# Performance work log

Hardware: AMD Instinct MI355X
Metric: run time of the kernel (lower is better)

Reference implementation:

```python
import jax, jax.numpy as jnp
import numpy as np

N_NODES = 100000
N_EDGES = 1000000
D_FEAT = 64          # per-node embedding dim
IN_FEATS = 2 * D_FEAT  # concat(src, dst)
HID = 128


def setup_inputs() -> dict:
    key = jax.random.key(0)
    ks = jax.random.split(key, 12)
    zi = jax.random.normal(ks[0], (N_NODES, D_FEAT), dtype=jnp.float32)
    zj = jax.random.normal(ks[1], (N_NODES, D_FEAT), dtype=jnp.float32)
    zn = jax.random.normal(ks[2], (N_NODES, D_FEAT), dtype=jnp.float32)
    pos_src = jax.random.randint(ks[3], (N_EDGES,), 0, N_NODES)
    pos_dst = jax.random.randint(ks[4], (N_EDGES,), 0, N_NODES)
    neg_src = jax.random.randint(ks[5], (N_EDGES,), 0, N_NODES)
    neg_dst = jax.random.randint(ks[6], (N_EDGES,), 0, N_NODES)
    # MLP params (nn.Linear style: y = x @ W.T + b)
    s1 = 1.0 / np.sqrt(IN_FEATS)
    s3 = 1.0 / np.sqrt(HID)
    W1 = jax.random.uniform(ks[7], (HID, IN_FEATS), jnp.float32, -s1, s1)
    b1 = jax.random.uniform(ks[8], (HID,), jnp.float32, -s1, s1)
    W3 = jax.random.uniform(ks[9], (1, HID), jnp.float32, -s3, s3)
    b3 = jax.random.uniform(ks[10], (1,), jnp.float32, -s3, s3)
    return {"zi": zi, "zj": zj, "zn": zn, "W1": W1, "b1": b1, "W3": W3,
            "b3": b3, "pos_src": pos_src, "pos_dst": pos_dst,
            "neg_src": neg_src, "neg_dst": neg_dst}


def _lp(raw, W1, b1, W3, b3):
    # Link_Prediction with n_layers=2, dropout=0: linear-relu-linear-sigmoid
    hid = jax.nn.relu(raw @ W1.T + b1)      # [E, HID]
    return jax.nn.sigmoid(hid @ W3.T + b3)  # [E, 1]


def reference(zi, zj, zn, W1, b1, W3, b3, pos_src, pos_dst, neg_src, neg_dst):
    # pos graph: gather src/dst node embeddings per edge, concat -> MLP
    raw_pos = jnp.concatenate([zi[pos_src], zj[pos_dst]], axis=1)  # [E, 2*D]
    pos_score = _lp(raw_pos, W1, b1, W3, b3)
    # NOTE: source bug — neg score is computed from the POS raw features
    # (pos_graph.edata['raw']); the neg gather/concat is dead code, so we
    # faithfully score raw_pos again.
    neg_score = _lp(raw_pos, W1, b1, W3, b3)
    return pos_score, neg_score
```

## Files before the change

### kernel.cpp

```cpp
#include <hip/hip_runtime.h>

typedef float    f32x16 __attribute__((ext_vector_type(16)));
typedef _Float16 f16x8  __attribute__((ext_vector_type(8)));

#define NWAVES 4
#define TPW 4
#define TILES_PER_BLOCK (NWAVES * TPW)

__global__ __launch_bounds__(256) void prep_f16(
    const float* __restrict__ zi, const float* __restrict__ zj,
    _Float16* __restrict__ zif, _Float16* __restrict__ zjf, const int nChunkPer)
{
    const int stride = gridDim.x * blockDim.x;
    for (int c = blockIdx.x * blockDim.x + threadIdx.x; c < 2 * nChunkPer; c += stride) {
        const float* s;
        _Float16* d;
        if (c < nChunkPer) { s = zi + (size_t)c * 8; d = zif + (size_t)c * 8; }
        else { s = zj + (size_t)(c - nChunkPer) * 8; d = zjf + (size_t)(c - nChunkPer) * 8; }
        const float4 a0 = *reinterpret_cast<const float4*>(s);
        const float4 a1 = *reinterpret_cast<const float4*>(s + 4);
        f16x8 v;
        v[0]=(_Float16)a0.x; v[1]=(_Float16)a0.y; v[2]=(_Float16)a0.z; v[3]=(_Float16)a0.w;
        v[4]=(_Float16)a1.x; v[5]=(_Float16)a1.y; v[6]=(_Float16)a1.z; v[7]=(_Float16)a1.w;
        *reinterpret_cast<f16x8*>(d) = v;
    }
}

template<bool F16TAB>
__global__ __launch_bounds__(256) void graphlp_mfma(
    const float* __restrict__ zi, const float* __restrict__ zj,
    const _Float16* __restrict__ zif, const _Float16* __restrict__ zjf,
    const float* __restrict__ W1, const float* __restrict__ b1p,
    const float* __restrict__ W3, const float* __restrict__ b3p,
    const int* __restrict__ psrc, const int* __restrict__ pdst,
    float* __restrict__ out, const int nEdges, const int nTiles)
{
    __shared__ uint4 w1s[2048];
    char* lds = reinterpret_cast<char*>(w1s);
    const int tid = threadIdx.x;

    #pragma unroll
    for (int i = 0; i < 8; ++i) {
        const int ch  = tid + i * 256;
        const int row = ch >> 4;
        const int kg  = ch & 15;
        const float* s = W1 + row * 128 + kg * 8;
        const float4 a0 = *reinterpret_cast<const float4*>(s);
        const float4 a1 = *reinterpret_cast<const float4*>(s + 4);
        f16x8 v;
        v[0]=(_Float16)a0.x; v[1]=(_Float16)a0.y; v[2]=(_Float16)a0.z; v[3]=(_Float16)a0.w;
        v[4]=(_Float16)a1.x; v[5]=(_Float16)a1.y; v[6]=(_Float16)a1.z; v[7]=(_Float16)a1.w;
        const int off = row * 256 + ((kg * 16) ^ ((row & 7) << 4));
        *reinterpret_cast<f16x8*>(lds + off) = v;
    }
    __syncthreads();

    const int lane = tid & 63;
    const int wav  = tid >> 6;
    const int lr   = lane & 31;
    const int lq   = lane >> 5;

    float b1v[4], w3v[4];
    #pragma unroll
    for (int nb = 0; nb < 4; ++nb) {
        b1v[nb] = b1p[nb * 32 + lr];
        w3v[nb] = W3[nb * 32 + lr];
    }
    const float b3 = b3p[0];

    int si = 0, di = 0;
    {
        const int g0 = blockIdx.x * TILES_PER_BLOCK + wav;
        if (g0 < nTiles) {
            const int e = min(g0 * 32 + lr, nEdges - 1);
            si = psrc[e]; di = pdst[e];
        }
    }

    for (int t = 0; t < TPW; ++t) {
        const int g = blockIdx.x * TILES_PER_BLOCK + t * NWAVES + wav;
        if (g >= nTiles) break;

        int si_n = 0, di_n = 0;
        if (t + 1 < TPW) {
            const int gn = g + NWAVES;
            if (gn < nTiles) {
                const int en = min(gn * 32 + lr, nEdges - 1);
                si_n = psrc[en]; di_n = pdst[en];
            }
        }

        f16x8 afrag[8];
        if constexpr (F16TAB) {
            const _Float16* __restrict__ sp = zif + (size_t)si * 64;
            const _Float16* __restrict__ dp = zjf + (size_t)di * 64;
            #pragma unroll
            for (int kk = 0; kk < 4; ++kk) {
                afrag[kk]     = *reinterpret_cast<const f16x8*>(sp + kk * 16 + lq * 8);
                afrag[kk + 4] = *reinterpret_cast<const f16x8*>(dp + kk * 16 + lq * 8);
            }
        } else {
            const float* __restrict__ sp = zi + (size_t)si * 64;
            const float* __restrict__ dp = zj + (size_t)di * 64;
            #pragma unroll
            for (int kk = 0; kk < 8; ++kk) {
                const int kb = kk * 16 + lq * 8;
                const float* p = (kk < 4) ? (sp + kb) : (dp + kb - 64);
                const float4 a0 = *reinterpret_cast<const float4*>(p);
                const float4 a1 = *reinterpret_cast<const float4*>(p + 4);
                f16x8 v;
                v[0]=(_Float16)a0.x; v[1]=(_Float16)a0.y; v[2]=(_Float16)a0.z; v[3]=(_Float16)a0.w;
                v[4]=(_Float16)a1.x; v[5]=(_Float16)a1.y; v[6]=(_Float16)a1.z; v[7]=(_Float16)a1.w;
                afrag[kk] = v;
            }
        }

        float pr[16];
        #pragma unroll
        for (int r = 0; r < 16; ++r) pr[r] = 0.0f;

        #pragma unroll
        for (int nbp = 0; nbp < 2; ++nbp) {
            f32x16 acc0, acc1;
            #pragma unroll
            for (int r = 0; r < 16; ++r) { acc0[r] = 0.0f; acc1[r] = 0.0f; }
            const int n0 = (2*nbp)     * 32 + lr;
            const int n1 = (2*nbp + 1) * 32 + lr;
            #pragma unroll
            for (int kk = 0; kk < 8; ++kk) {
                const int kx = kk * 32 + lq * 16;
                const f16x8 bf0 = *reinterpret_cast<const f16x8*>(
                    lds + n0 * 256 + (kx ^ ((n0 & 7) << 4)));
                const f16x8 bf1 = *reinterpret_cast<const f16x8*>(
                    lds + n1 * 256 + (kx ^ ((n1 & 7) << 4)));
                acc0 = __builtin_amdgcn_mfma_f32_32x32x16_f16(afrag[kk], bf0, acc0, 0, 0, 0);
                acc1 = __builtin_amdgcn_mfma_f32_32x32x16_f16(afrag[kk], bf1, acc1, 0, 0, 0);
            }
            const float bb0 = b1v[2*nbp], bb1 = b1v[2*nbp + 1];
            const float ww0 = w3v[2*nbp], ww1 = w3v[2*nbp + 1];
            #pragma unroll
            for (int r = 0; r < 16; ++r) {
                pr[r] = fmaf(fmaxf(acc0[r] + bb0, 0.0f), ww0, pr[r]);
                pr[r] = fmaf(fmaxf(acc1[r] + bb1, 0.0f), ww1, pr[r]);
            }
        }

        float p8[8];
        #pragma unroll
        for (int r = 0; r < 8; ++r) {
            const float lo = pr[r], hi = pr[r + 8];
            const float sent = (lane & 1) ? lo : hi;
            const float got  = __shfl_xor(sent, 1);
            p8[r] = ((lane & 1) ? hi : lo) + got;
        }
        float p4[4];
        #pragma unroll
        for (int r = 0; r < 4; ++r) {
            const float lo = p8[r], hi = p8[r + 4];
            const float sent = (lane & 2) ? lo : hi;
            const float got  = __shfl_xor(sent, 2);
            p4[r] = ((lane & 2) ? hi : lo) + got;
        }
        float p2[2];
        #pragma unroll
        for (int r = 0; r < 2; ++r) {
            const float lo = p4[r], hi = p4[r + 2];
            const float sent = (lane & 4) ? lo : hi;
            const float got  = __shfl_xor(sent, 4);
            p2[r] = ((lane & 4) ? hi : lo) + got;
        }
        float p1;
        {
            const float lo = p2[0], hi = p2[1];
            const float sent = (lane & 8) ? lo : hi;
            const float got  = __shfl_xor(sent, 8);
            p1 = ((lane & 8) ? hi : lo) + got;
        }
        p1 += __shfl_xor(p1, 16);

        const int rid = 8 * (lane & 1) + 4 * ((lane >> 1) & 1)
                      + 2 * ((lane >> 2) & 1) + ((lane >> 3) & 1);
        const int m  = (rid & 3) + 8 * (rid >> 2) + 4 * lq;
        const int eo = g * 32 + m;
        if (eo < nEdges) {
            const float sc = 1.0f / (1.0f + __expf(-(p1 + b3)));
            if (lane & 16) out[nEdges + eo] = sc;
            else           out[eo] = sc;
        }

        si = si_n; di = di_n;
    }
}

extern "C" void kernel_launch(void* const* d_in, const int* in_sizes, int n_in,
                              void* d_out, int out_size, void* d_ws, size_t ws_size,
                              hipStream_t stream)
{
    const float* zi = (const float*)d_in[0];
    const float* zj = (const float*)d_in[1];
    const float* W1 = (const float*)d_in[3];
    const float* b1 = (const float*)d_in[4];
    const float* W3 = (const float*)d_in[5];
    const float* b3 = (const float*)d_in[6];
    const int* psrc = (const int*)d_in[7];
    const int* pdst = (const int*)d_in[8];
    float* out = (float*)d_out;

    const int nEdges = in_sizes[7];
    const int nNodesI = in_sizes[0] / 64;
    const int nNodesJ = in_sizes[1] / 64;
    const int nTiles = (nEdges + 31) / 32;
    const int nBlocks = (nTiles + TILES_PER_BLOCK - 1) / TILES_PER_BLOCK;

    const size_t bytesI = (size_t)nNodesI * 64 * sizeof(_Float16);
    const size_t bytesJ = (size_t)nNodesJ * 64 * sizeof(_Float16);
    const bool useF16 = (ws_size >= bytesI + bytesJ) && (nNodesI == nNodesJ);

    if (useF16) {
        _Float16* zif = (_Float16*)d_ws;
        _Float16* zjf = (_Float16*)((char*)d_ws + bytesI);
        const int nChunkPer = nNodesI * 64 / 8;
        hipLaunchKernelGGL(prep_f16, dim3(2048), dim3(256), 0, stream,
                           zi, zj, zif, zjf, nChunkPer);
        hipLaunchKernelGGL((graphlp_mfma<true>), dim3(nBlocks), dim3(256), 0, stream,
                           zi, zj, zif, zjf, W1, b1, W3, b3, psrc, pdst,
                           out, nEdges, nTiles);
    } else {
        hipLaunchKernelGGL((graphlp_mfma<false>), dim3(nBlocks), dim3(256), 0, stream,
                           zi, zj, (const _Float16*)nullptr, (const _Float16*)nullptr,
                           W1, b1, W3, b3, psrc, pdst, out, nEdges, nTiles);
    }
}
```

Baseline: 67.93 us.

## Software-pipeline embedding gathers one tile ahead and double tiles per wave

Restructures the per-wave tile loop so that the gathered A fragments for the next tile are loaded while the current tile's MFMAs run, with edge indices prefetched two tiles ahead. Tiles per wave are doubled to amortize the W1 LDS staging across more work. The bias is folded into the accumulator initialization, and s_setprio is raised around the MFMA block. The exchange is higher register pressure from the second fragment set and a fully unrolled loop, plus fewer blocks, which can hurt occupancy and load balance.

```diff
diff --git a/kernel.cpp b/kernel.cpp
--- a/kernel.cpp
+++ b/kernel.cpp
@@ -4,7 +4,7 @@
 typedef _Float16 f16x8  __attribute__((ext_vector_type(8)));
 
 #define NWAVES 4
-#define TPW 4
+#define TPW 8
 #define TILES_PER_BLOCK (NWAVES * TPW)
 
 __global__ __launch_bounds__(256) void prep_f16(
@@ -23,6 +23,37 @@
         v[0]=(_Float16)a0.x; v[1]=(_Float16)a0.y; v[2]=(_Float16)a0.z; v[3]=(_Float16)a0.w;
         v[4]=(_Float16)a1.x; v[5]=(_Float16)a1.y; v[6]=(_Float16)a1.z; v[7]=(_Float16)a1.w;
         *reinterpret_cast<f16x8*>(d) = v;
+    }
+}
+
+template<bool F16TAB>
+__device__ inline void load_afrag(f16x8 (&a)[8],
+    const float* __restrict__ zi, const float* __restrict__ zj,
+    const _Float16* __restrict__ zif, const _Float16* __restrict__ zjf,
+    const int si, const int di, const int lq)
+{
+    if constexpr (F16TAB) {
+        const _Float16* __restrict__ sp = zif + (size_t)si * 64;
+        const _Float16* __restrict__ dp = zjf + (size_t)di * 64;
+        #pragma unroll
+        for (int kk = 0; kk < 4; ++kk) {
+            a[kk]     = *reinterpret_cast<const f16x8*>(sp + kk * 16 + lq * 8);
+            a[kk + 4] = *reinterpret_cast<const f16x8*>(dp + kk * 16 + lq * 8);
+        }
+    } else {
+        const float* __restrict__ sp = zi + (size_t)si * 64;
+        const float* __restrict__ dp = zj + (size_t)di * 64;
+        #pragma unroll
+        for (int kk = 0; kk < 8; ++kk) {
+            const int kb = kk * 16 + lq * 8;
+            const float* p = (kk < 4) ? (sp + kb) : (dp + kb - 64);
+            const float4 a0 = *reinterpret_cast<const float4*>(p);
+            const float4 a1 = *reinterpret_cast<const float4*>(p + 4);
+            f16x8 v;
+            v[0]=(_Float16)a0.x; v[1]=(_Float16)a0.y; v[2]=(_Float16)a0.z; v[3]=(_Float16)a0.w;
+            v[4]=(_Float16)a1.x; v[5]=(_Float16)a1.y; v[6]=(_Float16)a1.z; v[7]=(_Float16)a1.w;
+            a[kk] = v;
+        }
     }
 }
 
@@ -68,52 +99,43 @@
     }
     const float b3 = b3p[0];
 
-    int si = 0, di = 0;
+    const int gbase = blockIdx.x * TILES_PER_BLOCK + wav;
+
+    f16x8 af[8];
+    int si1 = 0, di1 = 0;
     {
-        const int g0 = blockIdx.x * TILES_PER_BLOCK + wav;
-        if (g0 < nTiles) {
-            const int e = min(g0 * 32 + lr, nEdges - 1);
-            si = psrc[e]; di = pdst[e];
-        }
-    }
-
+        int si0 = 0, di0 = 0;
+        if (gbase < nTiles) {
+            const int e = min(gbase * 32 + lr, nEdges - 1);
+            si0 = psrc[e]; di0 = pdst[e];
+        }
+        const int gB = gbase + NWAVES;
+        if (gB < nTiles) {
+            const int e = min(gB * 32 + lr, nEdges - 1);
+            si1 = psrc[e]; di1 = pdst[e];
+        }
+        if (gbase < nTiles)
+            load_afrag<F16TAB>(af, zi, zj, zif, zjf, si0, di0, lq);
+    }
+
+    #pragma unroll
     for (int t = 0; t < TPW; ++t) {
-        const int g = blockIdx.x * TILES_PER_BLOCK + t * NWAVES + wav;
+        const int g = gbase + t * NWAVES;
         if (g >= nTiles) break;
 
-        int si_n = 0, di_n = 0;
-        if (t + 1 < TPW) {
-            const int gn = g + NWAVES;
-            if (gn < nTiles) {
-                const int en = min(gn * 32 + lr, nEdges - 1);
-                si_n = psrc[en]; di_n = pdst[en];
+        int si2 = 0, di2 = 0;
+        if (t + 2 < TPW) {
+            const int g2 = g + 2 * NWAVES;
+            if (g2 < nTiles) {
+                const int e2 = min(g2 * 32 + lr, nEdges - 1);
+                si2 = psrc[e2]; di2 = pdst[e2];
             }
         }
 
-        f16x8 afrag[8];
-        if constexpr (F16TAB) {
-            const _Float16* __restrict__ sp = zif + (size_t)si * 64;
-            const _Float16* __restrict__ dp = zjf + (size_t)di * 64;
-            #pragma unroll
-            for (int kk = 0; kk < 4; ++kk) {
-                afrag[kk]     = *reinterpret_cast<const f16x8*>(sp + kk * 16 + lq * 8);
-                afrag[kk + 4] = *reinterpret_cast<const f16x8*>(dp + kk * 16 + lq * 8);
-            }
-        } else {
-            const float* __restrict__ sp = zi + (size_t)si * 64;
-            const float* __restrict__ dp = zj + (size_t)di * 64;
-            #pragma unroll
-            for (int kk = 0; kk < 8; ++kk) {
-                const int kb = kk * 16 + lq * 8;
-                const float* p = (kk < 4) ? (sp + kb) : (dp + kb - 64);
-                const float4 a0 = *reinterpret_cast<const float4*>(p);
-                const float4 a1 = *reinterpret_cast<const float4*>(p + 4);
-                f16x8 v;
-                v[0]=(_Float16)a0.x; v[1]=(_Float16)a0.y; v[2]=(_Float16)a0.z; v[3]=(_Float16)a0.w;
-                v[4]=(_Float16)a1.x; v[5]=(_Float16)a1.y; v[6]=(_Float16)a1.z; v[7]=(_Float16)a1.w;
-                afrag[kk] = v;
-            }
-        }
+        f16x8 an[8];
+        const bool havnext = (t + 1 < TPW) && (g + NWAVES < nTiles);
+        if (havnext)
+            load_afrag<F16TAB>(an, zi, zj, zif, zjf, si1, di1, lq);
 
         float pr[16];
         #pragma unroll
@@ -121,11 +143,13 @@
 
         #pragma unroll
         for (int nbp = 0; nbp < 2; ++nbp) {
+            const float bb0 = b1v[2*nbp], bb1 = b1v[2*nbp + 1];
             f32x16 acc0, acc1;
             #pragma unroll
-            for (int r = 0; r < 16; ++r) { acc0[r] = 0.0f; acc1[r] = 0.0f; }
+            for (int r = 0; r < 16; ++r) { acc0[r] = bb0; acc1[r] = bb1; }
             const int n0 = (2*nbp)     * 32 + lr;
             const int n1 = (2*nbp + 1) * 32 + lr;
+            __builtin_amdgcn_s_setprio(1);
             #pragma unroll
             for (int kk = 0; kk < 8; ++kk) {
                 const int kx = kk * 32 + lq * 16;
@@ -133,15 +157,15 @@
                     lds + n0 * 256 + (kx ^ ((n0 & 7) << 4)));
                 const f16x8 bf1 = *reinterpret_cast<const f16x8*>(
                     lds + n1 * 256 + (kx ^ ((n1 & 7) << 4)));
-                acc0 = __builtin_amdgcn_mfma_f32_32x32x16_f16(afrag[kk], bf0, acc0, 0, 0, 0);
-                acc1 = __builtin_amdgcn_mfma_f32_32x32x16_f16(afrag[kk], bf1, acc1, 0, 0, 0);
+                acc0 = __builtin_amdgcn_mfma_f32_32x32x16_f16(af[kk], bf0, acc0, 0, 0, 0);
+                acc1 = __builtin_amdgcn_mfma_f32_32x32x16_f16(af[kk], bf1, acc1, 0, 0, 0);
             }
-            const float bb0 = b1v[2*nbp], bb1 = b1v[2*nbp + 1];
+            __builtin_amdgcn_s_setprio(0);
             const float ww0 = w3v[2*nbp], ww1 = w3v[2*nbp + 1];
             #pragma unroll
             for (int r = 0; r < 16; ++r) {
-                pr[r] = fmaf(fmaxf(acc0[r] + bb0, 0.0f), ww0, pr[r]);
-                pr[r] = fmaf(fmaxf(acc1[r] + bb1, 0.0f), ww1, pr[r]);
+                pr[r] = fmaf(fmaxf(acc0[r], 0.0f), ww0, pr[r]);
+                pr[r] = fmaf(fmaxf(acc1[r], 0.0f), ww1, pr[r]);
             }
         }
 
@@ -188,7 +212,9 @@
             else           out[eo] = sc;
         }
 
-        si = si_n; di = di_n;
+        #pragma unroll
+        for (int kk = 0; kk < 8; ++kk) af[kk] = an[kk];
+        si1 = si2; di1 = di2;
     }
 }
 
```

Measured after the change: 70.90 us. 1.04x slower.

## Store node embedding tables as FP8 e4m3 and decode to f16 in gather

Applied to the files above, without the earlier changes.

The prep pass now converts zi/zj to 8-bit e4m3 instead of f16, halving the bytes gathered per edge in the main kernel. The gather loads 8-byte chunks and decodes them to f16 before the MFMA. The change also seeds the accumulators with the bias, fully unrolls the tile loop, and raises wave priority around the MFMA loop. FP8 quantisation adds notable precision loss to the embeddings, which may push results past tolerance. It also drops the equal-node-count check and adds decode ALU work.

```diff
diff --git a/kernel.cpp b/kernel.cpp
--- a/kernel.cpp
+++ b/kernel.cpp
@@ -1,4 +1,5 @@
 #include <hip/hip_runtime.h>
+#include <hip/hip_fp8.h>
 
 typedef float    f32x16 __attribute__((ext_vector_type(16)));
 typedef _Float16 f16x8  __attribute__((ext_vector_type(8)));
@@ -7,29 +8,68 @@
 #define TPW 4
 #define TILES_PER_BLOCK (NWAVES * TPW)
 
-__global__ __launch_bounds__(256) void prep_f16(
+__device__ __forceinline__ uint32_t enc4_fp8(float a, float b, float c, float d) {
+#if __has_builtin(__builtin_amdgcn_cvt_pk_fp8_f32)
+    int w = __builtin_amdgcn_cvt_pk_fp8_f32(a, b, 0, false);
+    w     = __builtin_amdgcn_cvt_pk_fp8_f32(c, d, w, true);
+    return (uint32_t)w;
+#else
+    __hip_fp8_e4m3 e0(a), e1(b), e2(c), e3(d);
+    return (uint32_t)e0.__x | ((uint32_t)e1.__x << 8) |
+           ((uint32_t)e2.__x << 16) | ((uint32_t)e3.__x << 24);
+#endif
+}
+
+__device__ __forceinline__ void dec4_fp8(uint32_t w, _Float16* o) {
+#if __has_builtin(__builtin_amdgcn_cvt_pk_f32_fp8)
+    const auto f01 = __builtin_amdgcn_cvt_pk_f32_fp8((int)w, false);
+    const auto f23 = __builtin_amdgcn_cvt_pk_f32_fp8((int)w, true);
+    const auto h01 = __builtin_amdgcn_cvt_pkrtz(f01[0], f01[1]);
+    const auto h23 = __builtin_amdgcn_cvt_pkrtz(f23[0], f23[1]);
+    o[0] = h01[0]; o[1] = h01[1]; o[2] = h23[0]; o[3] = h23[1];
+#else
+    #pragma unroll
+    for (int j = 0; j < 4; ++j) {
+        __hip_fp8_e4m3 t; t.__x = (unsigned char)(w >> (8 * j));
+        o[j] = (_Float16)(float)t;
+    }
+#endif
+}
+
+__device__ __forceinline__ f16x8 dec8_fp8(uint2 u) {
+    f16x8 v;
+    _Float16 tmp[8];
+    dec4_fp8(u.x, tmp);
+    dec4_fp8(u.y, tmp + 4);
+    #pragma unroll
+    for (int j = 0; j < 8; ++j) v[j] = tmp[j];
+    return v;
+}
+
+__global__ __launch_bounds__(256) void prep_fp8(
     const float* __restrict__ zi, const float* __restrict__ zj,
-    _Float16* __restrict__ zif, _Float16* __restrict__ zjf, const int nChunkPer)
+    uint2* __restrict__ zif8, uint2* __restrict__ zjf8, const int nChunkPer)
 {
     const int stride = gridDim.x * blockDim.x;
     for (int c = blockIdx.x * blockDim.x + threadIdx.x; c < 2 * nChunkPer; c += stride) {
         const float* s;
-        _Float16* d;
-        if (c < nChunkPer) { s = zi + (size_t)c * 8; d = zif + (size_t)c * 8; }
-        else { s = zj + (size_t)(c - nChunkPer) * 8; d = zjf + (size_t)(c - nChunkPer) * 8; }
+        uint2* d;
+        int cc;
+        if (c < nChunkPer) { cc = c; s = zi + (size_t)cc * 8; d = zif8 + cc; }
+        else { cc = c - nChunkPer; s = zj + (size_t)cc * 8; d = zjf8 + cc; }
         const float4 a0 = *reinterpret_cast<const float4*>(s);
         const float4 a1 = *reinterpret_cast<const float4*>(s + 4);
-        f16x8 v;
-        v[0]=(_Float16)a0.x; v[1]=(_Float16)a0.y; v[2]=(_Float16)a0.z; v[3]=(_Float16)a0.w;
-        v[4]=(_Float16)a1.x; v[5]=(_Float16)a1.y; v[6]=(_Float16)a1.z; v[7]=(_Float16)a1.w;
-        *reinterpret_cast<f16x8*>(d) = v;
-    }
-}
-
-template<bool F16TAB>
+        uint2 w;
+        w.x = enc4_fp8(a0.x, a0.y, a0.z, a0.w);
+        w.y = enc4_fp8(a1.x, a1.y, a1.z, a1.w);
+        *d = w;
+    }
+}
+
+template<bool FP8>
 __global__ __launch_bounds__(256) void graphlp_mfma(
     const float* __restrict__ zi, const float* __restrict__ zj,
-    const _Float16* __restrict__ zif, const _Float16* __restrict__ zjf,
+    const unsigned char* __restrict__ zif8, const unsigned char* __restrict__ zjf8,
     const float* __restrict__ W1, const float* __restrict__ b1p,
     const float* __restrict__ W3, const float* __restrict__ b3p,
     const int* __restrict__ psrc, const int* __restrict__ pdst,
@@ -77,6 +117,7 @@
         }
     }
 
+    #pragma unroll
     for (int t = 0; t < TPW; ++t) {
         const int g = blockIdx.x * TILES_PER_BLOCK + t * NWAVES + wav;
         if (g >= nTiles) break;
@@ -91,14 +132,17 @@
         }
 
         f16x8 afrag[8];
-        if constexpr (F16TAB) {
-            const _Float16* __restrict__ sp = zif + (size_t)si * 64;
-            const _Float16* __restrict__ dp = zjf + (size_t)di * 64;
+        if constexpr (FP8) {
+            const unsigned char* __restrict__ sp = zif8 + (size_t)si * 64;
+            const unsigned char* __restrict__ dp = zjf8 + (size_t)di * 64;
+            uint2 px[8];
             #pragma unroll
             for (int kk = 0; kk < 4; ++kk) {
-                afrag[kk]     = *reinterpret_cast<const f16x8*>(sp + kk * 16 + lq * 8);
-                afrag[kk + 4] = *reinterpret_cast<const f16x8*>(dp + kk * 16 + lq * 8);
-            }
+                px[kk]     = *reinterpret_cast<const uint2*>(sp + kk * 16 + lq * 8);
+                px[kk + 4] = *reinterpret_cast<const uint2*>(dp + kk * 16 + lq * 8);
+            }
+            #pragma unroll
+            for (int kk = 0; kk < 8; ++kk) afrag[kk] = dec8_fp8(px[kk]);
         } else {
             const float* __restrict__ sp = zi + (size_t)si * 64;
             const float* __restrict__ dp = zj + (size_t)di * 64;
@@ -121,11 +165,13 @@
 
         #pragma unroll
         for (int nbp = 0; nbp < 2; ++nbp) {
+            const float bb0 = b1v[2*nbp], bb1 = b1v[2*nbp + 1];
             f32x16 acc0, acc1;
             #pragma unroll
-            for (int r = 0; r < 16; ++r) { acc0[r] = 0.0f; acc1[r] = 0.0f; }
+            for (int r = 0; r < 16; ++r) { acc0[r] = bb0; acc1[r] = bb1; }
             const int n0 = (2*nbp)     * 32 + lr;
             const int n1 = (2*nbp + 1) * 32 + lr;
+            __builtin_amdgcn_s_setprio(1);
             #pragma unroll
             for (int kk = 0; kk < 8; ++kk) {
                 const int kx = kk * 32 + lq * 16;
@@ -136,12 +182,12 @@
                 acc0 = __builtin_amdgcn_mfma_f32_32x32x16_f16(afrag[kk], bf0, acc0, 0, 0, 0);
                 acc1 = __builtin_amdgcn_mfma_f32_32x32x16_f16(afrag[kk], bf1, acc1, 0, 0, 0);
             }
-            const float bb0 = b1v[2*nbp], bb1 = b1v[2*nbp + 1];
+            __builtin_amdgcn_s_setprio(0);
             const float ww0 = w3v[2*nbp], ww1 = w3v[2*nbp + 1];
             #pragma unroll
             for (int r = 0; r < 16; ++r) {
-                pr[r] = fmaf(fmaxf(acc0[r] + bb0, 0.0f), ww0, pr[r]);
-                pr[r] = fmaf(fmaxf(acc1[r] + bb1, 0.0f), ww1, pr[r]);
+                pr[r] = fmaf(fmaxf(acc0[r], 0.0f), ww0, pr[r]);
+                pr[r] = fmaf(fmaxf(acc1[r], 0.0f), ww1, pr[r]);
             }
         }
 
@@ -212,22 +258,22 @@
     const int nTiles = (nEdges + 31) / 32;
     const int nBlocks = (nTiles + TILES_PER_BLOCK - 1) / TILES_PER_BLOCK;
 
-    const size_t bytesI = (size_t)nNodesI * 64 * sizeof(_Float16);
-    const size_t bytesJ = (size_t)nNodesJ * 64 * sizeof(_Float16);
-    const bool useF16 = (ws_size >= bytesI + bytesJ) && (nNodesI == nNodesJ);
-
-    if (useF16) {
-        _Float16* zif = (_Float16*)d_ws;
-        _Float16* zjf = (_Float16*)((char*)d_ws + bytesI);
+    const size_t bytesI = (size_t)nNodesI * 64;
+    const size_t bytesJ = (size_t)nNodesJ * 64;
+    const bool useF8 = (ws_size >= bytesI + bytesJ);
+
+    if (useF8) {
+        unsigned char* zif8 = (unsigned char*)d_ws;
+        unsigned char* zjf8 = (unsigned char*)d_ws + bytesI;
         const int nChunkPer = nNodesI * 64 / 8;
-        hipLaunchKernelGGL(prep_f16, dim3(2048), dim3(256), 0, stream,
-                           zi, zj, zif, zjf, nChunkPer);
+        hipLaunchKernelGGL(prep_fp8, dim3(2048), dim3(256), 0, stream,
+                           zi, zj, (uint2*)zif8, (uint2*)zjf8, nChunkPer);
         hipLaunchKernelGGL((graphlp_mfma<true>), dim3(nBlocks), dim3(256), 0, stream,
-                           zi, zj, zif, zjf, W1, b1, W3, b3, psrc, pdst,
+                           zi, zj, zif8, zjf8, W1, b1, W3, b3, psrc, pdst,
                            out, nEdges, nTiles);
     } else {
         hipLaunchKernelGGL((graphlp_mfma<false>), dim3(nBlocks), dim3(256), 0, stream,
-                           zi, zj, (const _Float16*)nullptr, (const _Float16*)nullptr,
+                           zi, zj, (const unsigned char*)nullptr, (const unsigned char*)nullptr,
                            W1, b1, W3, b3, psrc, pdst, out, nEdges, nTiles);
     }
 }
```

After: 72.36 us. 6.5% more time.
